# Kernel optimization log

Measured on AMD Instinct MI355X. Metric: run time of the kernel, lower is better.

Reference implementation:

```python
import jax, jax.numpy as jnp
import numpy as np

B, S, D = 2, 512, 256

def setup_inputs() -> dict:
    key = jax.random.key(0)
    k1, k2, k3, k4, k5 = jax.random.split(key, 5)
    return {
        "query": jax.random.normal(k1, (B, S, D), dtype=jnp.float32),
        "key": jax.random.normal(k2, (B, S, D), dtype=jnp.float32),
        "value": jax.random.normal(k3, (B, S, D), dtype=jnp.float32),
        "Wm_w": jax.random.normal(k4, (D, D), dtype=jnp.float32) * (1.0 / np.sqrt(D)),
        "vm_w": jax.random.normal(k5, (1, D), dtype=jnp.float32) * (1.0 / np.sqrt(D)),
    }

def reference(query, key, value, Wm_w, vm_w):
    # pairwise difference: q.unsqueeze(1) - q.unsqueeze(2) -> [B, S, S, D]
    diff = query[:, None, :, :] - query[:, :, None, :]
    # Wm (Linear, no bias): [B,S,S,D] @ Wm_w^T, then tanh
    h = jnp.tanh(jnp.einsum('bijd,ed->bije', diff, Wm_w))
    # vm (Linear D->1, no bias) + squeeze -> scores [B, S, S]
    sjt = jnp.einsum('bije,e->bij', h, vm_w[0])
    # softmax over dim=2 (eval mode: dropout is identity)
    atten = jax.nn.softmax(sjt, axis=2)
    # bmm(atten, value) -> [B, S, D]
    context = jnp.einsum('bij,bjd->bid', atten, value)
    return context, atten
```

## Files before the change

### kernel.cpp

```cpp
#include <hip/hip_runtime.h>

#define B 2
#define S 512
#define D 256
#define C2L 2.885390081777927f
#define LOG2E 1.4426950408889634f

__global__ __launch_bounds__(256) void proj_kernel(const float* __restrict__ q,
                                                   const float* __restrict__ W,
                                                   float* __restrict__ EJ,
                                                   float* __restrict__ P) {
    __shared__ float qlds[4 * D];
    const int t = threadIdx.x;
    const int b = blockIdx.x / (S / 4);
    const int i0 = (blockIdx.x % (S / 4)) * 4;
    const float* qbase = q + (size_t)(b * S + i0) * D;
    for (int idx = t; idx < 4 * D; idx += 256) qlds[idx] = qbase[idx];
    __syncthreads();
    const float* wr = W + (size_t)t * D;
    float a0 = 0.f, a1 = 0.f, a2 = 0.f, a3 = 0.f;
#pragma unroll 4
    for (int d = 0; d < D; ++d) {
        float w = wr[d];
        a0 = fmaf(qlds[d], w, a0);
        a1 = fmaf(qlds[D + d], w, a1);
        a2 = fmaf(qlds[2 * D + d], w, a2);
        a3 = fmaf(qlds[3 * D + d], w, a3);
    }
    a0 *= C2L; a1 *= C2L; a2 *= C2L; a3 *= C2L;
    float* ej = EJ + (size_t)(b * D + t) * S + i0;
    *(float4*)ej = make_float4(__builtin_amdgcn_exp2f(a0), __builtin_amdgcn_exp2f(a1),
                               __builtin_amdgcn_exp2f(a2), __builtin_amdgcn_exp2f(a3));
    P[(size_t)(b * S + i0 + 0) * D + t] = a0;
    P[(size_t)(b * S + i0 + 1) * D + t] = a1;
    P[(size_t)(b * S + i0 + 2) * D + t] = a2;
    P[(size_t)(b * S + i0 + 3) * D + t] = a3;
}

__global__ __launch_bounds__(1024) void score_kernel(const float* __restrict__ EJ,
                                                     const float* __restrict__ P,
                                                     const float* __restrict__ vm,
                                                     float* __restrict__ sc) {
    __shared__ float4 fA[D], fB[D];
    __shared__ float2 comb[2][S];
    __shared__ float cred[16];

    const int t = threadIdx.x;
    const int b = blockIdx.x >> 7;
    const int m = blockIdx.x & 127;
    const int r0 = 2 * m, r1 = r0 + 1;
    const int q0 = 510 - 2 * m, q1 = q0 + 1;
    const int segA = 511 - 2 * m;

    float pc = 0.f;
    if (t < D) {
        const size_t bP = (size_t)b * S * D;
        float v = vm[t];
        pc = v;
        fA[t] = make_float4(__builtin_amdgcn_exp2f(-P[bP + (size_t)r0 * D + t]),
                            __builtin_amdgcn_exp2f(-P[bP + (size_t)r1 * D + t]),
                            -2.f * v, 0.f);
        fB[t] = make_float4(__builtin_amdgcn_exp2f(-P[bP + (size_t)q0 * D + t]),
                            __builtin_amdgcn_exp2f(-P[bP + (size_t)q1 * D + t]),
                            -2.f * v, 0.f);
    }
#pragma unroll
    for (int off = 32; off; off >>= 1) pc += __shfl_xor(pc, off);
    if ((t & 63) == 0) cred[t >> 6] = pc;
    __syncthreads();
    float c = 0.f;
#pragma unroll
    for (int wv = 0; wv < 16; ++wv) c += cred[wv];

    const int eh = t >> 9;
    const int s = t & 511;
    const bool inA = s < segA;
    const int j = inA ? (r0 + 1 + s) : s;
    const float4* ff = inA ? fA : fB;
    const float* ej = EJ + (size_t)b * D * S + j;

    float a0 = 0.f, a1 = 0.f;
    const int e0 = eh * 128;
#pragma unroll 8
    for (int e = e0; e < e0 + 128; ++e) {
        float ev = ej[(size_t)e * S];
        float4 f = ff[e];
        float x0 = ev * f.x;
        float x1 = ev * f.y;
        float y0 = 1.f + x0;
        float y1 = 1.f + x1;
        float rv = __builtin_amdgcn_rcpf(y0);
        float rn = __uint_as_float(0x7EF311C3u - __float_as_uint(y1));
        rn = rn * fmaf(-y1, rn, 2.f);
        rn = rn * fmaf(-y1, rn, 2.f);
        a0 = fmaf(f.z, rv, a0);
        a1 = fmaf(f.z, rn, a1);
    }
    comb[eh][s] = make_float2(a0, a1);
    __syncthreads();

    float* sb = sc + (size_t)b * S * S;
    {
        float2 vL = comb[0][s], vH = comb[1][s];
        float d0 = vL.x + vH.x, d1 = vL.y + vH.y;
        const int rr0 = inA ? r0 : q0;
        const int rr1 = inA ? r1 : q1;
        if (eh == 0) {
            sb[(size_t)rr0 * S + j] = d0;
            sb[(size_t)rr1 * S + j] = d1;
        } else {
            *(float2*)&sb[(size_t)j * S + rr0] =
                make_float2(fmaf(-2.f, c, -d0), fmaf(-2.f, c, -d1));
        }
    }
    if (t < 2) {
        const int rr = (t == 0) ? r0 : q0;
        sb[(size_t)rr * S + rr] = -c;
    }
}

__global__ __launch_bounds__(512) void softctx_kernel(float* __restrict__ att,
                                                      const float* __restrict__ value,
                                                      float* __restrict__ ctx) {
    __shared__ float a4[S][4];
    __shared__ float part[4][8][64][4];
    __shared__ float redm[4][2], reds[4][2];

    const int t = threadIdx.x;
    const int b = blockIdx.x >> 7;
    const int i0 = (blockIdx.x & 127) * 4;

    {
        const int row = t >> 7, jr = t & 127;
        const int lane = t & 63, half = (t >> 6) & 1;
        float* arow = att + (size_t)(b * S + i0 + row) * S;
        float s0 = arow[jr], s1 = arow[jr + 128], s2 = arow[jr + 256], s3 = arow[jr + 384];
        float lm = fmaxf(fmaxf(s0, s1), fmaxf(s2, s3));
#pragma unroll
        for (int off = 32; off; off >>= 1) lm = fmaxf(lm, __shfl_xor(lm, off));
        if (lane == 0) redm[row][half] = lm;
        __syncthreads();
        float m = fmaxf(redm[row][0], redm[row][1]);
        float p0 = __builtin_amdgcn_exp2f((s0 - m) * LOG2E);
        float p1 = __builtin_amdgcn_exp2f((s1 - m) * LOG2E);
        float p2 = __builtin_amdgcn_exp2f((s2 - m) * LOG2E);
        float p3 = __builtin_amdgcn_exp2f((s3 - m) * LOG2E);
        float ls = (p0 + p1) + (p2 + p3);
#pragma unroll
        for (int off = 32; off; off >>= 1) ls += __shfl_xor(ls, off);
        if (lane == 0) reds[row][half] = ls;
        __syncthreads();
        float rinv = __builtin_amdgcn_rcpf(reds[row][0] + reds[row][1]);
        p0 *= rinv; p1 *= rinv; p2 *= rinv; p3 *= rinv;
        arow[jr] = p0; arow[jr + 128] = p1; arow[jr + 256] = p2; arow[jr + 384] = p3;
        a4[jr][row] = p0; a4[jr + 128][row] = p1;
        a4[jr + 256][row] = p2; a4[jr + 384][row] = p3;
    }
    __syncthreads();

    {
        const int dq = t & 63, js = t >> 6;
        float4 acc0 = {}, acc1 = {}, acc2 = {}, acc3 = {};
        const float* vb = value + (size_t)b * S * D + (size_t)dq * 4;
#pragma unroll 4
        for (int jj = 0; jj < 64; ++jj) {
            int j = js * 64 + jj;
            float4 v = *(const float4*)(vb + (size_t)j * D);
            float w0 = a4[j][0], w1 = a4[j][1], w2 = a4[j][2], w3 = a4[j][3];
            acc0.x = fmaf(w0, v.x, acc0.x); acc0.y = fmaf(w0, v.y, acc0.y);
            acc0.z = fmaf(w0, v.z, acc0.z); acc0.w = fmaf(w0, v.w, acc0.w);
            acc1.x = fmaf(w1, v.x, acc1.x); acc1.y = fmaf(w1, v.y, acc1.y);
            acc1.z = fmaf(w1, v.z, acc1.z); acc1.w = fmaf(w1, v.w, acc1.w);
            acc2.x = fmaf(w2, v.x, acc2.x); acc2.y = fmaf(w2, v.y, acc2.y);
            acc2.z = fmaf(w2, v.z, acc2.z); acc2.w = fmaf(w2, v.w, acc2.w);
            acc3.x = fmaf(w3, v.x, acc3.x); acc3.y = fmaf(w3, v.y, acc3.y);
            acc3.z = fmaf(w3, v.z, acc3.z); acc3.w = fmaf(w3, v.w, acc3.w);
        }
        *(float4*)&part[0][js][dq][0] = acc0;
        *(float4*)&part[1][js][dq][0] = acc1;
        *(float4*)&part[2][js][dq][0] = acc2;
        *(float4*)&part[3][js][dq][0] = acc3;
    }
    __syncthreads();
    if (t < 256) {
        const int row = t >> 6, dq = t & 63;
        float4 sum = {};
#pragma unroll
        for (int js = 0; js < 8; ++js) {
            float4 p = *(const float4*)&part[row][js][dq][0];
            sum.x += p.x; sum.y += p.y; sum.z += p.z; sum.w += p.w;
        }
        *(float4*)(ctx + (size_t)(b * S + i0 + row) * D + (size_t)dq * 4) = sum;
    }
}

extern "C" void kernel_launch(void* const* d_in, const int* in_sizes, int n_in,
                              void* d_out, int out_size, void* d_ws, size_t ws_size,
                              hipStream_t stream) {
    const float* q = (const float*)d_in[0];
    const float* value = (const float*)d_in[2];
    const float* W = (const float*)d_in[3];
    const float* vm = (const float*)d_in[4];

    float* ctx = (float*)d_out;
    float* att = ctx + (size_t)B * S * D;
    float* EJ = (float*)d_ws;
    float* P = EJ + (size_t)B * D * S;

    proj_kernel<<<B * (S / 4), 256, 0, stream>>>(q, W, EJ, P);
    score_kernel<<<B * 128, 1024, 0, stream>>>(EJ, P, vm, att);
    softctx_kernel<<<B * (S / 4), 512, 0, stream>>>(att, value, ctx);
}
```

Measured before the change: 41.74 us.

## Split score kernel across e-halves into separate blocks with partial score buffers

The score kernel now launches 512-thread blocks, twice as many as before. Each block handles one half of the e dimension and writes partial scores to a two-slice workspace buffer. The softmax kernel sums the two slices, which removes the in-block combine and the 1024-thread blocks. The proj kernel also precomputes exp2(-P), so score blocks load it directly instead of exponentiating. The cost is more workspace traffic: two partial score matrices are written and then read back.

```diff
diff --git a/kernel.cpp b/kernel.cpp
--- a/kernel.cpp
+++ b/kernel.cpp
@@ -9,7 +9,7 @@
 __global__ __launch_bounds__(256) void proj_kernel(const float* __restrict__ q,
                                                    const float* __restrict__ W,
                                                    float* __restrict__ EJ,
-                                                   float* __restrict__ P) {
+                                                   float* __restrict__ EN) {
     __shared__ float qlds[4 * D];
     const int t = threadIdx.x;
     const int b = blockIdx.x / (S / 4);
@@ -31,96 +31,84 @@
     float* ej = EJ + (size_t)(b * D + t) * S + i0;
     *(float4*)ej = make_float4(__builtin_amdgcn_exp2f(a0), __builtin_amdgcn_exp2f(a1),
                                __builtin_amdgcn_exp2f(a2), __builtin_amdgcn_exp2f(a3));
-    P[(size_t)(b * S + i0 + 0) * D + t] = a0;
-    P[(size_t)(b * S + i0 + 1) * D + t] = a1;
-    P[(size_t)(b * S + i0 + 2) * D + t] = a2;
-    P[(size_t)(b * S + i0 + 3) * D + t] = a3;
-}
-
-__global__ __launch_bounds__(1024) void score_kernel(const float* __restrict__ EJ,
-                                                     const float* __restrict__ P,
-                                                     const float* __restrict__ vm,
-                                                     float* __restrict__ sc) {
-    __shared__ float4 fA[D], fB[D];
-    __shared__ float2 comb[2][S];
-    __shared__ float cred[16];
+    EN[(size_t)(b * S + i0 + 0) * D + t] = __builtin_amdgcn_exp2f(-a0);
+    EN[(size_t)(b * S + i0 + 1) * D + t] = __builtin_amdgcn_exp2f(-a1);
+    EN[(size_t)(b * S + i0 + 2) * D + t] = __builtin_amdgcn_exp2f(-a2);
+    EN[(size_t)(b * S + i0 + 3) * D + t] = __builtin_amdgcn_exp2f(-a3);
+}
+
+__global__ __launch_bounds__(512, 4) void score_kernel(const float* __restrict__ EJ,
+                                                       const float* __restrict__ EN,
+                                                       const float* __restrict__ vm,
+                                                       float* __restrict__ sc) {
+    __shared__ float fpair[2][128][2];
+    __shared__ float wl[128];
+    __shared__ float cred[8];
 
     const int t = threadIdx.x;
-    const int b = blockIdx.x >> 7;
-    const int m = blockIdx.x & 127;
-    const int r0 = 2 * m, r1 = r0 + 1;
-    const int q0 = 510 - 2 * m, q1 = q0 + 1;
-    const int segA = 511 - 2 * m;
-
+    const int bid = blockIdx.x;
+    const int b = bid >> 8;
+    const int m = bid & 255;
+    const int eh = m & 1;
+    const int mm = m >> 1;
+    const int e0 = eh * 128;
+    const int r0 = 2 * mm;
+    const int q0 = 510 - 2 * mm;
+
+    {
+        const int rr = t >> 7, el = t & 127;
+        const int row = ((rr < 2) ? r0 : q0) + (rr & 1);
+        fpair[rr >> 1][el][rr & 1] = EN[((size_t)b * S + row) * D + e0 + el];
+    }
     float pc = 0.f;
-    if (t < D) {
-        const size_t bP = (size_t)b * S * D;
-        float v = vm[t];
+    if (t < 128) {
+        float v = vm[e0 + t];
+        wl[t] = -2.f * v;
         pc = v;
-        fA[t] = make_float4(__builtin_amdgcn_exp2f(-P[bP + (size_t)r0 * D + t]),
-                            __builtin_amdgcn_exp2f(-P[bP + (size_t)r1 * D + t]),
-                            -2.f * v, 0.f);
-        fB[t] = make_float4(__builtin_amdgcn_exp2f(-P[bP + (size_t)q0 * D + t]),
-                            __builtin_amdgcn_exp2f(-P[bP + (size_t)q1 * D + t]),
-                            -2.f * v, 0.f);
     }
 #pragma unroll
     for (int off = 32; off; off >>= 1) pc += __shfl_xor(pc, off);
     if ((t & 63) == 0) cred[t >> 6] = pc;
     __syncthreads();
-    float c = 0.f;
-#pragma unroll
-    for (int wv = 0; wv < 16; ++wv) c += cred[wv];
-
-    const int eh = t >> 9;
-    const int s = t & 511;
-    const bool inA = s < segA;
-    const int j = inA ? (r0 + 1 + s) : s;
-    const float4* ff = inA ? fA : fB;
-    const float* ej = EJ + (size_t)b * D * S + j;
+    float ch = 0.f;
+#pragma unroll
+    for (int wv = 0; wv < 8; ++wv) ch += cred[wv];
+
+    const int segA = 511 - 2 * mm;
+    const bool inA = t < segA;
+    const int j = inA ? (r0 + 1 + t) : t;
+    const int rb0 = inA ? r0 : q0;
+    const float2* fp = (const float2*)&fpair[inA ? 0 : 1][0][0];
+    const float* ejp = EJ + ((size_t)b * D + e0) * S + j;
 
     float a0 = 0.f, a1 = 0.f;
-    const int e0 = eh * 128;
 #pragma unroll 8
-    for (int e = e0; e < e0 + 128; ++e) {
-        float ev = ej[(size_t)e * S];
-        float4 f = ff[e];
-        float x0 = ev * f.x;
-        float x1 = ev * f.y;
-        float y0 = 1.f + x0;
-        float y1 = 1.f + x1;
+    for (int el = 0; el < 128; ++el) {
+        float ev = ejp[(size_t)el * S];
+        float2 f = fp[el];
+        float w = wl[el];
+        float y0 = fmaf(ev, f.x, 1.f);
+        float y1 = fmaf(ev, f.y, 1.f);
         float rv = __builtin_amdgcn_rcpf(y0);
         float rn = __uint_as_float(0x7EF311C3u - __float_as_uint(y1));
         rn = rn * fmaf(-y1, rn, 2.f);
         rn = rn * fmaf(-y1, rn, 2.f);
-        a0 = fmaf(f.z, rv, a0);
-        a1 = fmaf(f.z, rn, a1);
-    }
-    comb[eh][s] = make_float2(a0, a1);
-    __syncthreads();
-
-    float* sb = sc + (size_t)b * S * S;
-    {
-        float2 vL = comb[0][s], vH = comb[1][s];
-        float d0 = vL.x + vH.x, d1 = vL.y + vH.y;
-        const int rr0 = inA ? r0 : q0;
-        const int rr1 = inA ? r1 : q1;
-        if (eh == 0) {
-            sb[(size_t)rr0 * S + j] = d0;
-            sb[(size_t)rr1 * S + j] = d1;
-        } else {
-            *(float2*)&sb[(size_t)j * S + rr0] =
-                make_float2(fmaf(-2.f, c, -d0), fmaf(-2.f, c, -d1));
-        }
-    }
-    if (t < 2) {
-        const int rr = (t == 0) ? r0 : q0;
-        sb[(size_t)rr * S + rr] = -c;
-    }
-}
-
-__global__ __launch_bounds__(512) void softctx_kernel(float* __restrict__ att,
+        a0 = fmaf(w, rv, a0);
+        a1 = fmaf(w, rn, a1);
+    }
+
+    float* sb = sc + ((size_t)eh * B + b) * S * S;
+    sb[(size_t)rb0 * S + j] = a0;
+    sb[(size_t)(rb0 + 1) * S + j] = a1;
+    *(float2*)&sb[(size_t)j * S + rb0] =
+        make_float2(fmaf(-2.f, ch, -a0), fmaf(-2.f, ch, -a1));
+    if (t == 0) sb[(size_t)r0 * S + r0] = -ch;
+    if (t == 1) sb[(size_t)q0 * S + q0] = -ch;
+}
+
+__global__ __launch_bounds__(512) void softctx_kernel(const float* __restrict__ sc,
                                                       const float* __restrict__ value,
+                                                      float* __restrict__ att,
                                                       float* __restrict__ ctx) {
     __shared__ float a4[S][4];
     __shared__ float part[4][8][64][4];
@@ -133,8 +121,12 @@
     {
         const int row = t >> 7, jr = t & 127;
         const int lane = t & 63, half = (t >> 6) & 1;
-        float* arow = att + (size_t)(b * S + i0 + row) * S;
-        float s0 = arow[jr], s1 = arow[jr + 128], s2 = arow[jr + 256], s3 = arow[jr + 384];
+        const float* s0r = sc + (size_t)(b * S + i0 + row) * S;
+        const float* s1r = s0r + (size_t)B * S * S;
+        float s0 = s0r[jr] + s1r[jr];
+        float s1 = s0r[jr + 128] + s1r[jr + 128];
+        float s2 = s0r[jr + 256] + s1r[jr + 256];
+        float s3 = s0r[jr + 384] + s1r[jr + 384];
         float lm = fmaxf(fmaxf(s0, s1), fmaxf(s2, s3));
 #pragma unroll
         for (int off = 32; off; off >>= 1) lm = fmaxf(lm, __shfl_xor(lm, off));
@@ -152,6 +144,7 @@
         __syncthreads();
         float rinv = __builtin_amdgcn_rcpf(reds[row][0] + reds[row][1]);
         p0 *= rinv; p1 *= rinv; p2 *= rinv; p3 *= rinv;
+        float* arow = att + (size_t)(b * S + i0 + row) * S;
         arow[jr] = p0; arow[jr + 128] = p1; arow[jr + 256] = p2; arow[jr + 384] = p3;
         a4[jr][row] = p0; a4[jr + 128][row] = p1;
         a4[jr + 256][row] = p2; a4[jr + 384][row] = p3;
@@ -205,9 +198,10 @@
     float* ctx = (float*)d_out;
     float* att = ctx + (size_t)B * S * D;
     float* EJ = (float*)d_ws;
-    float* P = EJ + (size_t)B * D * S;
-
-    proj_kernel<<<B * (S / 4), 256, 0, stream>>>(q, W, EJ, P);
-    score_kernel<<<B * 128, 1024, 0, stream>>>(EJ, P, vm, att);
-    softctx_kernel<<<B * (S / 4), 512, 0, stream>>>(att, value, ctx);
-}
+    float* EN = EJ + (size_t)B * D * S;
+    float* SC = EN + (size_t)B * S * D;
+
+    proj_kernel<<<B * (S / 4), 256, 0, stream>>>(q, W, EJ, EN);
+    score_kernel<<<B * 256, 512, 0, stream>>>(EJ, EN, vm, SC);
+    softctx_kernel<<<B * (S / 4), 512, 0, stream>>>(SC, value, att, ctx);
+}
```

Measured after the change: 41.60 us. About the same (-0.3%).
